# Kernel optimization log

Hardware: AMD Instinct MI355X
Metric: run time of the kernel (lower is better)

Reference implementation:

```python
import jax, jax.numpy as jnp
import numpy as np
import math

N_HEAD = 16
N_EMBED = 1024
BLOCK_SIZE = 2048


def setup_inputs() -> dict:
    key = jax.random.key(0)
    k0, k1, k2, k3, k4 = jax.random.split(key, 5)
    B, T, C = 2, 2048, N_EMBED
    x = jax.random.normal(k0, (B, T, C), dtype=jnp.float32)
    # torch nn.Linear weights: [out_features, in_features]
    s_attn = 1.0 / math.sqrt(C)
    W_attn = jax.random.uniform(k1, (3 * C, C), dtype=jnp.float32, minval=-s_attn, maxval=s_attn)
    b_attn = jax.random.uniform(k2, (3 * C,), dtype=jnp.float32, minval=-s_attn, maxval=s_attn)
    W_proj = jax.random.uniform(k3, (C, C), dtype=jnp.float32, minval=-s_attn, maxval=s_attn)
    b_proj = jax.random.uniform(k4, (C,), dtype=jnp.float32, minval=-s_attn, maxval=s_attn)
    return {"x": x, "W_attn": W_attn, "b_attn": b_attn, "W_proj": W_proj, "b_proj": b_proj}


def reference(x, W_attn, b_attn, W_proj, b_proj):
    B, T, C = x.shape
    H = N_HEAD
    D = C // H
    qkv = x @ W_attn.T + b_attn                     # [B,T,3C]
    q, k, v = jnp.split(qkv, 3, axis=2)
    # [B,T,C] -> [B,H,T,D]
    q = q.reshape(B, T, H, D).transpose(0, 2, 1, 3)
    k = k.reshape(B, T, H, D).transpose(0, 2, 1, 3)
    v = v.reshape(B, T, H, D).transpose(0, 2, 1, 3)
    scale = 1.0 / math.sqrt(D)
    attn = jnp.einsum('bhqd,bhkd->bhqk', q, k) * scale   # [B,H,T,T]
    causal = jnp.tril(jnp.ones((T, T), dtype=bool))
    attn = jnp.where(causal[None, None, :, :], attn, -jnp.inf)
    attn = jax.nn.softmax(attn, axis=-1)
    y = jnp.einsum('bhqk,bhkd->bhqd', attn, v)           # [B,H,T,D]
    y = y.transpose(0, 2, 1, 3).reshape(B, T, C)
    return y @ W_proj.T + b_proj
```

## Files before the change

### kernel.cpp

```cpp
#include <hip/hip_runtime.h>
#include <hip/hip_bf16.h>

#define B_  2
#define T_  2048
#define C_  1024
#define H_  16
#define D_  64
#define M_  (B_*T_)
#define N1_ (3*C_)

typedef short bf16x8 __attribute__((ext_vector_type(8)));
typedef short bf16x4 __attribute__((ext_vector_type(4)));
typedef float f32x4 __attribute__((ext_vector_type(4)));
typedef unsigned short u16;
typedef u16 u16x8 __attribute__((ext_vector_type(8)));

#define QSCALE 0.18033688011112042f
#define C8     11.541560327111707f

__device__ __forceinline__ u16 f2bf(float f) {
  unsigned u = __float_as_uint(f);
  u += 0x7FFFu + ((u >> 16) & 1u);
  return (u16)(u >> 16);
}

__device__ __forceinline__ void gload16(const void* g, void* l) {
  __builtin_amdgcn_global_load_lds((__attribute__((address_space(1))) void*)g,
                                   (__attribute__((address_space(3))) void*)l,
                                   16, 0, 0);
}

__global__ __launch_bounds__(256) void cvt3(const float* __restrict__ x,
                                            const float* __restrict__ wa,
                                            const float* __restrict__ wp,
                                            u16* __restrict__ out) {
  int i = (blockIdx.x * 256 + threadIdx.x) * 8;
  const float* src;
  int off;
  if (i < M_ * C_)                 { src = x;  off = 0; }
  else if (i < M_ * C_ + N1_ * C_) { src = wa; off = M_ * C_; }
  else                             { src = wp; off = M_ * C_ + N1_ * C_; }
  float4 a = *(const float4*)(src + (i - off));
  float4 b = *(const float4*)(src + (i - off) + 4);
  u16x8 o;
  o[0] = f2bf(a.x); o[1] = f2bf(a.y); o[2] = f2bf(a.z); o[3] = f2bf(a.w);
  o[4] = f2bf(b.x); o[5] = f2bf(b.y); o[6] = f2bf(b.z); o[7] = f2bf(b.w);
  *(u16x8*)(out + i) = o;
}

__device__ __forceinline__ void gemm_core(const u16* __restrict__ A,
                                          const u16* __restrict__ W,
                                          u16* As, u16* Bs,
                                          f32x4 (&acc)[4][4],
                                          int m0, int n0, int K) {
  int tid = threadIdx.x;
  int lane = tid & 63, wid = tid >> 6;
  int wr = wid >> 1, wc = wid & 1;

  int arow = wid * 16 + (lane >> 2);
  int ag = lane & 3;
  int sg = ag ^ ((arow >> 1) & 3);
  const u16* aSrc0 = A + (m0 + arow) * K + sg * 8;
  const u16* aSrc1 = aSrc0 + 64 * K;
  const u16* bSrc0 = W + (n0 + arow) * K + sg * 8;
  const u16* bSrc1 = bSrc0 + 64 * K;
  u16* aDst0 = As + (wid * 16) * 32;
  u16* aDst1 = As + (64 + wid * 16) * 32;
  u16* bDst0 = Bs + (wid * 16) * 32;
  u16* bDst1 = Bs + (64 + wid * 16) * 32;

  int rg = lane >> 4;
  int aoff[4], boff[4];
#pragma unroll
  for (int m = 0; m < 4; ++m) {
    int row = wr * 64 + m * 16 + (lane & 15);
    aoff[m] = row * 32 + (rg ^ ((row >> 1) & 3)) * 8;
    row = wc * 64 + m * 16 + (lane & 15);
    boff[m] = row * 32 + (rg ^ ((row >> 1) & 3)) * 8;
  }

  for (int kt = 0; kt < K / 32; ++kt) {
    int k0 = kt * 32;
    __syncthreads();
    gload16(aSrc0 + k0, aDst0);
    gload16(aSrc1 + k0, aDst1);
    gload16(bSrc0 + k0, bDst0);
    gload16(bSrc1 + k0, bDst1);
    __syncthreads();

    bf16x8 af[4], bfr[4];
#pragma unroll
    for (int m = 0; m < 4; ++m) af[m] = *(const bf16x8*)(As + aoff[m]);
#pragma unroll
    for (int n = 0; n < 4; ++n) bfr[n] = *(const bf16x8*)(Bs + boff[n]);
#pragma unroll
    for (int m = 0; m < 4; ++m)
#pragma unroll
      for (int n = 0; n < 4; ++n)
        acc[m][n] = __builtin_amdgcn_mfma_f32_16x16x32_bf16(af[m], bfr[n], acc[m][n], 0, 0, 0);
  }
}

__global__ __launch_bounds__(256) void gemm_qkv(const u16* __restrict__ A,
                                                const u16* __restrict__ W,
                                                const float* __restrict__ bias,
                                                u16* __restrict__ Qb,
                                                u16* __restrict__ Kb,
                                                u16* __restrict__ Vt) {
  __shared__ __align__(16) u16 As[128 * 32];
  __shared__ __align__(16) u16 Bs[128 * 32];
  f32x4 acc[4][4] = {};
  int m0 = blockIdx.x * 128, n0 = blockIdx.y * 128;
  gemm_core(A, W, As, Bs, acc, m0, n0, C_);

  int lane = threadIdx.x & 63, wid = threadIdx.x >> 6;
  int wr = wid >> 1, wc = wid & 1;
  int rg = lane >> 4, cl = lane & 15;
#pragma unroll
  for (int n = 0; n < 4; ++n) {
    int gn = n0 + wc * 64 + n * 16 + cl;
    float bv = bias[gn];
    int seg = gn >> 10, cc = gn & 1023;
    int h = cc >> 6, d = cc & 63;
    float sc = (seg == 0) ? QSCALE : 1.0f;
#pragma unroll
    for (int m = 0; m < 4; ++m) {
#pragma unroll
      for (int r = 0; r < 4; ++r) {
        int gm = m0 + wr * 64 + m * 16 + rg * 4 + r;
        int b = gm >> 11, t = gm & 2047;
        u16 val = f2bf((acc[m][n][r] + bv) * sc);
        int bh = b * 16 + h;
        if (seg == 0)      Qb[(bh * 2048 + t) * 64 + d] = val;
        else if (seg == 1) Kb[(bh * 2048 + t) * 64 + d] = val;
        else               Vt[(bh * 64 + d) * 2048 + t] = val;
      }
    }
  }
}

__global__ __launch_bounds__(256) void gemm_proj(const u16* __restrict__ A,
                                                 const u16* __restrict__ W,
                                                 const float* __restrict__ bias,
                                                 float* __restrict__ out) {
  __shared__ __align__(16) u16 As[128 * 32];
  __shared__ __align__(16) u16 Bs[128 * 32];
  f32x4 acc[4][4] = {};
  int m0 = blockIdx.x * 128, n0 = blockIdx.y * 128;
  gemm_core(A, W, As, Bs, acc, m0, n0, C_);

  int lane = threadIdx.x & 63, wid = threadIdx.x >> 6;
  int wr = wid >> 1, wc = wid & 1;
  int rg = lane >> 4, cl = lane & 15;
#pragma unroll
  for (int n = 0; n < 4; ++n) {
    int gn = n0 + wc * 64 + n * 16 + cl;
    float bv = bias[gn];
#pragma unroll
    for (int m = 0; m < 4; ++m) {
#pragma unroll
      for (int r = 0; r < 4; ++r) {
        int gm = m0 + wr * 64 + m * 16 + rg * 4 + r;
        out[gm * 1024 + gn] = acc[m][n][r] + bv;
      }
    }
  }
}

__global__ __launch_bounds__(128, 2) void attn_fwd(const u16* __restrict__ Qb,
                                                   const u16* __restrict__ Kb,
                                                   const u16* __restrict__ Vt,
                                                   u16* __restrict__ Yb) {
  __shared__ __align__(16) u16 Ps[2][32 * 64];
  __shared__ __align__(16) f32x4 Co[8][64];
  __shared__ float Cl[2][64];
  int tid = threadIdx.x, lane = tid & 63, wid = tid >> 6;
  int cl = lane & 15, kg = lane >> 4;
  int bid = blockIdx.x;
  int bh = bid & 31;
  int qwi = 63 - (bid >> 5);
  int qw0 = qwi * 32;
  int jmax = qwi >> 1;
  int fc0 = wid * 2;
  const u16* Qp = Qb + (size_t)bh * (2048 * 64);
  const u16* Kp = Kb + (size_t)bh * (2048 * 64);
  const u16* Vp = Vt + (size_t)bh * (64 * 2048);
  u16* Pw = Ps[wid];

  int kbase = cl * 64 + kg * 8 + fc0 * 1024;
  int vbase = cl * 2048 + wid * 32 + kg * 8;

  bf16x8 qf[2][2];
#pragma unroll
  for (int fr = 0; fr < 2; ++fr)
#pragma unroll
    for (int dk = 0; dk < 2; ++dk)
      qf[fr][dk] = *(const bf16x8*)(Qp + (qw0 + fr * 16 + cl) * 64 + dk * 32 + kg * 8);

  f32x4 o[2][4] = {};
  float lsum[2] = {0.f, 0.f};
  const f32x4 CINIT = {-C8, -C8, -C8, -C8};

  auto LOADK = [&](bf16x8 (&kf)[2][2], int j) {
    const u16* Kj = Kp + j * 4096 + kbase;
#pragma unroll
    for (int fcl = 0; fcl < 2; ++fcl) {
      kf[fcl][0] = *(const bf16x8*)(Kj + fcl * 1024);
      kf[fcl][1] = *(const bf16x8*)(Kj + fcl * 1024 + 32);
    }
  };

  auto LOADV = [&](bf16x8 (&vf)[4], int j) {
    const u16* Vj = Vp + j * 64 + vbase;
#pragma unroll
    for (int dc = 0; dc < 4; ++dc)
      vf[dc] = *(const bf16x8*)(Vj + dc * 32768);
  };

  auto CORE = [&](bf16x8 (&kf)[2][2], bf16x8 (&vf)[4], int j, bool edge) {
    f32x4 s[2][2];
#pragma unroll
    for (int fcl = 0; fcl < 2; ++fcl)
#pragma unroll
      for (int fr = 0; fr < 2; ++fr) {
        f32x4 z = CINIT;
        z = __builtin_amdgcn_mfma_f32_16x16x32_bf16(kf[fcl][0], qf[fr][0], z, 0, 0, 0);
        z = __builtin_amdgcn_mfma_f32_16x16x32_bf16(kf[fcl][1], qf[fr][1], z, 0, 0, 0);
        s[fr][fcl] = z;
      }
    if (edge) {
#pragma unroll
      for (int fr = 0; fr < 2; ++fr) {
        int qg = qw0 + fr * 16 + cl;
#pragma unroll
        for (int fcl = 0; fcl < 2; ++fcl)
#pragma unroll
          for (int r = 0; r < 4; ++r)
            if (j * 64 + (fc0 + fcl) * 16 + kg * 4 + r > qg) s[fr][fcl][r] = -1e30f;
      }
    }

#pragma unroll
    for (int fr = 0; fr < 2; ++fr) {
      int rowb = (fr * 16 + cl) * 64;
#pragma unroll
      for (int fcl = 0; fcl < 2; ++fcl) {
        float p0 = exp2f(s[fr][fcl][0]);
        float p1 = exp2f(s[fr][fcl][1]);
        float p2 = exp2f(s[fr][fcl][2]);
        float p3 = exp2f(s[fr][fcl][3]);
        lsum[fr] += (p0 + p1) + (p2 + p3);
        union { bf16x4 v; __hip_bfloat162 h[2]; } pk;
        pk.h[0] = __float22bfloat162_rn(make_float2(p0, p1));
        pk.h[1] = __float22bfloat162_rn(make_float2(p2, p3));
        int fc = fc0 + fcl;
        *(bf16x4*)(Pw + rowb + (((fc * 2 + (kg >> 1)) ^ (cl & 7)) * 8) + (kg & 1) * 4) = pk.v;
      }
    }
#pragma unroll
    for (int fr = 0; fr < 2; ++fr) {
      int rowb = (fr * 16 + cl) * 64;
      bf16x8 pf = *(const bf16x8*)(Pw + rowb + (((wid * 4 + kg) ^ (cl & 7)) * 8));
#pragma unroll
      for (int dc = 0; dc < 4; ++dc)
        o[fr][dc] = __builtin_amdgcn_mfma_f32_16x16x32_bf16(pf, vf[dc], o[fr][dc], 0, 0, 0);
    }
  };

  bool edgeMine = (fc0 <= ((qwi & 1) ? 3 : 1));

  bf16x8 kA[2][2], kB[2][2], vA[4], vB[4];
  LOADK(kA, 0); LOADV(vA, 0);
  if (jmax == 0) {
    if (edgeMine) CORE(kA, vA, 0, true);
  } else {
    LOADK(kB, 1); LOADV(vB, 1);
    int j = 0;
    while (j + 1 < jmax) {
      CORE(kA, vA, j, false);
      LOADK(kA, j + 2); LOADV(vA, j + 2);
      CORE(kB, vB, j + 1, false);
      int nx = (j + 3 <= jmax) ? j + 3 : jmax;
      LOADK(kB, nx); LOADV(vB, nx);
      j += 2;
    }
    if (j < jmax) { CORE(kA, vA, j, false); if (edgeMine) CORE(kB, vB, jmax, true); }
    else          { if (edgeMine) CORE(kA, vA, jmax, true); }
  }

  if (wid == 1) {
#pragma unroll
    for (int fr = 0; fr < 2; ++fr) {
      Cl[fr][lane] = lsum[fr];
#pragma unroll
      for (int dc = 0; dc < 4; ++dc) Co[fr * 4 + dc][lane] = o[fr][dc];
    }
  }
  __syncthreads();
  if (wid == 0) {
    int b = bh >> 4, h = bh & 15;
#pragma unroll
    for (int fr = 0; fr < 2; ++fr) {
      float l = lsum[fr] + Cl[fr][lane];
#pragma unroll
      for (int dc = 0; dc < 4; ++dc) o[fr][dc] += Co[fr * 4 + dc][lane];
      l += __shfl_xor(l, 16);
      l += __shfl_xor(l, 32);
      float linv = 1.f / l;
      float li[4];
#pragma unroll
      for (int r = 0; r < 4; ++r) li[r] = __shfl(linv, kg * 4 + r);
#pragma unroll
      for (int dc = 0; dc < 4; ++dc)
#pragma unroll
        for (int r = 0; r < 4; ++r) {
          int t = qw0 + fr * 16 + kg * 4 + r;
          int d = dc * 16 + cl;
          Yb[((size_t)(b * 2048 + t)) * 1024 + h * 64 + d] = f2bf(o[fr][dc][r] * li[r]);
        }
    }
  }
}

extern "C" void kernel_launch(void* const* d_in, const int* in_sizes, int n_in,
                              void* d_out, int out_size, void* d_ws, size_t ws_size,
                              hipStream_t stream) {
  const float* x  = (const float*)d_in[0];
  const float* Wa = (const float*)d_in[1];
  const float* ba = (const float*)d_in[2];
  const float* Wp = (const float*)d_in[3];
  const float* bp = (const float*)d_in[4];
  float* out = (float*)d_out;

  u16* xb  = (u16*)d_ws;
  u16* Wab = xb  + (size_t)M_ * C_;
  u16* Wpb = Wab + (size_t)N1_ * C_;
  u16* Qb  = Wpb + (size_t)C_ * C_;
  u16* Kb  = Qb  + (size_t)M_ * C_;
  u16* Vt  = Kb  + (size_t)M_ * C_;
  u16* Yb  = Vt  + (size_t)M_ * C_;

  cvt3<<<(M_ * C_ + N1_ * C_ + C_ * C_) / 2048, 256, 0, stream>>>(x, Wa, Wp, xb);
  gemm_qkv<<<dim3(M_ / 128, N1_ / 128), 256, 0, stream>>>(xb, Wab, ba, Qb, Kb, Vt);
  attn_fwd<<<2048, 128, 0, stream>>>(Qb, Kb, Vt, Yb);
  gemm_proj<<<dim3(M_ / 128, C_ / 128), 256, 0, stream>>>(Yb, Wpb, bp, out);
}
```

Measured before the change: 137.1 us.

## Split attention core into score/exp and PV phases with double-buffered P

```diff
diff --git a/kernel.cpp b/kernel.cpp
--- a/kernel.cpp
+++ b/kernel.cpp
@@ -171,7 +171,7 @@
                                                    const u16* __restrict__ Kb,
                                                    const u16* __restrict__ Vt,
                                                    u16* __restrict__ Yb) {
-  __shared__ __align__(16) u16 Ps[2][32 * 64];
+  __shared__ __align__(16) u16 Ps[2][2][32 * 64];
   __shared__ __align__(16) f32x4 Co[8][64];
   __shared__ float Cl[2][64];
   int tid = threadIdx.x, lane = tid & 63, wid = tid >> 6;
@@ -185,7 +185,8 @@
   const u16* Qp = Qb + (size_t)bh * (2048 * 64);
   const u16* Kp = Kb + (size_t)bh * (2048 * 64);
   const u16* Vp = Vt + (size_t)bh * (64 * 2048);
-  u16* Pw = Ps[wid];
+  u16* P0 = Ps[wid][0];
+  u16* P1 = Ps[wid][1];
 
   int kbase = cl * 64 + kg * 8 + fc0 * 1024;
   int vbase = cl * 2048 + wid * 32 + kg * 8;
@@ -217,7 +218,7 @@
       vf[dc] = *(const bf16x8*)(Vj + dc * 32768);
   };
 
-  auto CORE = [&](bf16x8 (&kf)[2][2], bf16x8 (&vf)[4], int j, bool edge) {
+  auto SEXP = [&](bf16x8 (&kf)[2][2], int j, bool edge, u16* Pw) {
     f32x4 s[2][2];
 #pragma unroll
     for (int fcl = 0; fcl < 2; ++fcl)
@@ -239,7 +240,6 @@
             if (j * 64 + (fc0 + fcl) * 16 + kg * 4 + r > qg) s[fr][fcl][r] = -1e30f;
       }
     }
-
 #pragma unroll
     for (int fr = 0; fr < 2; ++fr) {
       int rowb = (fr * 16 + cl) * 64;
@@ -257,6 +257,9 @@
         *(bf16x4*)(Pw + rowb + (((fc * 2 + (kg >> 1)) ^ (cl & 7)) * 8) + (kg & 1) * 4) = pk.v;
       }
     }
+  };
+
+  auto PV = [&](bf16x8 (&vf)[4], u16* Pw) {
 #pragma unroll
     for (int fr = 0; fr < 2; ++fr) {
       int rowb = (fr * 16 + cl) * 64;
@@ -269,23 +272,30 @@
 
   bool edgeMine = (fc0 <= ((qwi & 1) ? 3 : 1));
 
-  bf16x8 kA[2][2], kB[2][2], vA[4], vB[4];
-  LOADK(kA, 0); LOADV(vA, 0);
-  if (jmax == 0) {
-    if (edgeMine) CORE(kA, vA, 0, true);
+  bf16x8 k0[2][2], k1[2][2], v0[4], v1[4];
+  LOADK(k0, 0);
+  if (jmax >= 1) LOADK(k1, 1);
+
+  int j = 0;
+  while (j + 1 < jmax) {
+    LOADV(v0, j);
+    LOADV(v1, j + 1);
+    SEXP(k0, j, false, P0);
+    SEXP(k1, j + 1, false, P1);
+    LOADK(k0, j + 2);
+    LOADK(k1, (j + 3 <= jmax) ? j + 3 : jmax);
+    PV(v0, P0);
+    PV(v1, P1);
+    j += 2;
+  }
+  if (j == jmax) {
+    if (edgeMine) { LOADV(v0, j); SEXP(k0, j, true, P0); PV(v0, P0); }
   } else {
-    LOADK(kB, 1); LOADV(vB, 1);
-    int j = 0;
-    while (j + 1 < jmax) {
-      CORE(kA, vA, j, false);
-      LOADK(kA, j + 2); LOADV(vA, j + 2);
-      CORE(kB, vB, j + 1, false);
-      int nx = (j + 3 <= jmax) ? j + 3 : jmax;
-      LOADK(kB, nx); LOADV(vB, nx);
-      j += 2;
-    }
-    if (j < jmax) { CORE(kA, vA, j, false); if (edgeMine) CORE(kB, vB, jmax, true); }
-    else          { if (edgeMine) CORE(kA, vA, jmax, true); }
+    LOADV(v0, j);
+    SEXP(k0, j, false, P0);
+    if (edgeMine) { LOADV(v1, j + 1); SEXP(k1, j + 1, true, P1); }
+    PV(v0, P0);
+    if (edgeMine) PV(v1, P1);
   }
 
   if (wid == 1) {
```

Measured after the change: 136.8 us. Within noise of the previous version (-0.2%).

## Share LDS-staged K/V tiles across four query groups in attention kernel

Applied to the files above, without the earlier changes.

```diff
diff --git a/kernel.cpp b/kernel.cpp
--- a/kernel.cpp
+++ b/kernel.cpp
@@ -60,10 +60,10 @@
   int arow = wid * 16 + (lane >> 2);
   int ag = lane & 3;
   int sg = ag ^ ((arow >> 1) & 3);
-  const u16* aSrc0 = A + (m0 + arow) * K + sg * 8;
-  const u16* aSrc1 = aSrc0 + 64 * K;
-  const u16* bSrc0 = W + (n0 + arow) * K + sg * 8;
-  const u16* bSrc1 = bSrc0 + 64 * K;
+  const u16* aSrc0 = A + (size_t)(m0 + arow) * K + sg * 8;
+  const u16* aSrc1 = aSrc0 + (size_t)64 * K;
+  const u16* bSrc0 = W + (size_t)(n0 + arow) * K + sg * 8;
+  const u16* bSrc1 = bSrc0 + (size_t)64 * K;
   u16* aDst0 = As + (wid * 16) * 32;
   u16* aDst1 = As + (64 + wid * 16) * 32;
   u16* bDst0 = Bs + (wid * 16) * 32;
@@ -131,9 +131,9 @@
         int b = gm >> 11, t = gm & 2047;
         u16 val = f2bf((acc[m][n][r] + bv) * sc);
         int bh = b * 16 + h;
-        if (seg == 0)      Qb[(bh * 2048 + t) * 64 + d] = val;
-        else if (seg == 1) Kb[(bh * 2048 + t) * 64 + d] = val;
-        else               Vt[(bh * 64 + d) * 2048 + t] = val;
+        if (seg == 0)      Qb[((size_t)(bh * 2048 + t)) * 64 + d] = val;
+        else if (seg == 1) Kb[((size_t)(bh * 2048 + t)) * 64 + d] = val;
+        else               Vt[((size_t)(bh * 64 + d)) * 2048 + t] = val;
       }
     }
   }
@@ -161,63 +161,73 @@
 #pragma unroll
       for (int r = 0; r < 4; ++r) {
         int gm = m0 + wr * 64 + m * 16 + rg * 4 + r;
-        out[gm * 1024 + gn] = acc[m][n][r] + bv;
-      }
-    }
-  }
-}
-
-__global__ __launch_bounds__(128, 2) void attn_fwd(const u16* __restrict__ Qb,
+        out[(size_t)gm * 1024 + gn] = acc[m][n][r] + bv;
+      }
+    }
+  }
+}
+
+__global__ __launch_bounds__(512, 2) void attn_fwd(const u16* __restrict__ Qb,
                                                    const u16* __restrict__ Kb,
                                                    const u16* __restrict__ Vt,
                                                    u16* __restrict__ Yb) {
-  __shared__ __align__(16) u16 Ps[2][32 * 64];
-  __shared__ __align__(16) f32x4 Co[8][64];
-  __shared__ float Cl[2][64];
-  int tid = threadIdx.x, lane = tid & 63, wid = tid >> 6;
+  __shared__ __align__(16) u16 Ks[2][64 * 64];
+  __shared__ __align__(16) u16 Vs[2][64 * 64];
+  __shared__ __align__(16) u16 Ps[8][32 * 32];
+  int tid = threadIdx.x, lane = tid & 63, w = tid >> 6;
+  int w4 = w >> 1, kvh = w & 1;
   int cl = lane & 15, kg = lane >> 4;
+  int sw = (cl ^ (cl >> 2)) & 3;
   int bid = blockIdx.x;
   int bh = bid & 31;
-  int qwi = 63 - (bid >> 5);
-  int qw0 = qwi * 32;
-  int jmax = qwi >> 1;
-  int fc0 = wid * 2;
+  int i = bid >> 5;
+  int qt = (i < 8) ? i : 23 - i;
+  int qb0 = qt * 128 + w4 * 32;
+  int jmaxw = (qb0 + 31) >> 6;
+  int jmaxb = 2 * qt + 1;
+  bool hasHigh = (qb0 & 32) != 0;
   const u16* Qp = Qb + (size_t)bh * (2048 * 64);
   const u16* Kp = Kb + (size_t)bh * (2048 * 64);
   const u16* Vp = Vt + (size_t)bh * (64 * 2048);
-  u16* Pw = Ps[wid];
-
-  int kbase = cl * 64 + kg * 8 + fc0 * 1024;
-  int vbase = cl * 2048 + wid * 32 + kg * 8;
+  u16* Pw = Ps[w];
+
+  int srow8 = lane >> 3;
+  int sg = (lane & 7) ^ srow8;
+  const u16* Ksrc = Kp + (w * 8 + srow8) * 64 + sg * 8;
+  const u16* Vsrc = Vp + (w * 8 + srow8) * 2048 + sg * 8;
 
   bf16x8 qf[2][2];
 #pragma unroll
   for (int fr = 0; fr < 2; ++fr)
 #pragma unroll
     for (int dk = 0; dk < 2; ++dk)
-      qf[fr][dk] = *(const bf16x8*)(Qp + (qw0 + fr * 16 + cl) * 64 + dk * 32 + kg * 8);
+      qf[fr][dk] = *(const bf16x8*)(Qp + (qb0 + fr * 16 + cl) * 64 + dk * 32 + kg * 8);
 
   f32x4 o[2][4] = {};
   float lsum[2] = {0.f, 0.f};
   const f32x4 CINIT = {-C8, -C8, -C8, -C8};
 
-  auto LOADK = [&](bf16x8 (&kf)[2][2], int j) {
-    const u16* Kj = Kp + j * 4096 + kbase;
+  auto STAGE = [&](int j, int buf) {
+    gload16(Ksrc + j * 4096, &Ks[buf][w * 512]);
+    gload16(Vsrc + j * 64, &Vs[buf][w * 512]);
+  };
+
+  auto CORE = [&](int buf, int j, bool mask) {
+    const u16* Kl = Ks[buf];
+    const u16* Vl = Vs[buf];
+    bf16x8 kf[2][2];
 #pragma unroll
     for (int fcl = 0; fcl < 2; ++fcl) {
-      kf[fcl][0] = *(const bf16x8*)(Kj + fcl * 1024);
-      kf[fcl][1] = *(const bf16x8*)(Kj + fcl * 1024 + 32);
-    }
-  };
-
-  auto LOADV = [&](bf16x8 (&vf)[4], int j) {
-    const u16* Vj = Vp + j * 64 + vbase;
-#pragma unroll
-    for (int dc = 0; dc < 4; ++dc)
-      vf[dc] = *(const bf16x8*)(Vj + dc * 32768);
-  };
-
-  auto CORE = [&](bf16x8 (&kf)[2][2], bf16x8 (&vf)[4], int j, bool edge) {
+      int row = (kvh * 2 + fcl) * 16 + cl;
+      kf[fcl][0] = *(const bf16x8*)(Kl + row * 64 + ((kg ^ (cl & 7)) * 8));
+      kf[fcl][1] = *(const bf16x8*)(Kl + row * 64 + (((4 + kg) ^ (cl & 7)) * 8));
+    }
+    bf16x8 vf[4];
+#pragma unroll
+    for (int dc = 0; dc < 4; ++dc) {
+      int row = dc * 16 + cl;
+      vf[dc] = *(const bf16x8*)(Vl + row * 64 + (((kvh * 4 + kg) ^ (cl & 7)) * 8));
+    }
     f32x4 s[2][2];
 #pragma unroll
     for (int fcl = 0; fcl < 2; ++fcl)
@@ -228,21 +238,20 @@
         z = __builtin_amdgcn_mfma_f32_16x16x32_bf16(kf[fcl][1], qf[fr][1], z, 0, 0, 0);
         s[fr][fcl] = z;
       }
-    if (edge) {
+    if (mask) {
 #pragma unroll
       for (int fr = 0; fr < 2; ++fr) {
-        int qg = qw0 + fr * 16 + cl;
+        int qg = qb0 + fr * 16 + cl;
 #pragma unroll
         for (int fcl = 0; fcl < 2; ++fcl)
 #pragma unroll
           for (int r = 0; r < 4; ++r)
-            if (j * 64 + (fc0 + fcl) * 16 + kg * 4 + r > qg) s[fr][fcl][r] = -1e30f;
-      }
-    }
-
+            if (j * 64 + (kvh * 2 + fcl) * 16 + kg * 4 + r > qg) s[fr][fcl][r] = -1e30f;
+      }
+    }
 #pragma unroll
     for (int fr = 0; fr < 2; ++fr) {
-      int rowb = (fr * 16 + cl) * 64;
+      int rowb = (fr * 16 + cl) * 32;
 #pragma unroll
       for (int fcl = 0; fcl < 2; ++fcl) {
         float p0 = exp2f(s[fr][fcl][0]);
@@ -253,57 +262,49 @@
         union { bf16x4 v; __hip_bfloat162 h[2]; } pk;
         pk.h[0] = __float22bfloat162_rn(make_float2(p0, p1));
         pk.h[1] = __float22bfloat162_rn(make_float2(p2, p3));
-        int fc = fc0 + fcl;
-        *(bf16x4*)(Pw + rowb + (((fc * 2 + (kg >> 1)) ^ (cl & 7)) * 8) + (kg & 1) * 4) = pk.v;
-      }
-    }
+        *(bf16x4*)(Pw + rowb + (((fcl * 2 + (kg >> 1)) ^ sw) * 8) + (kg & 1) * 4) = pk.v;
+      }
+    }
+    bf16x8 pf[2];
+#pragma unroll
+    for (int fr = 0; fr < 2; ++fr)
+      pf[fr] = *(const bf16x8*)(Pw + (fr * 16 + cl) * 32 + ((kg ^ sw) * 8));
+#pragma unroll
+    for (int fr = 0; fr < 2; ++fr)
+#pragma unroll
+      for (int dc = 0; dc < 4; ++dc)
+        o[fr][dc] = __builtin_amdgcn_mfma_f32_16x16x32_bf16(pf[fr], vf[dc], o[fr][dc], 0, 0, 0);
+  };
+
+  STAGE(0, 0);
+  __syncthreads();
+  int buf = 0;
+  for (int j = 0; j <= jmaxb; ++j) {
+    if (j < jmaxb) STAGE(j + 1, buf ^ 1);
+    if (j < jmaxw)       CORE(buf, j, false);
+    else if (j == jmaxw && (kvh == 0 || hasHigh)) CORE(buf, j, true);
+    __syncthreads();
+    buf ^= 1;
+  }
+
+  f32x4* Co = (f32x4*)((w4 < 2) ? (void*)&Ks[0][0] : (void*)&Vs[0][0]) + (w4 & 1) * 512;
+  float*  Cl = (float*)&Ps[0][0] + w4 * 128;
+  if (kvh == 1) {
 #pragma unroll
     for (int fr = 0; fr < 2; ++fr) {
-      int rowb = (fr * 16 + cl) * 64;
-      bf16x8 pf = *(const bf16x8*)(Pw + rowb + (((wid * 4 + kg) ^ (cl & 7)) * 8));
-#pragma unroll
-      for (int dc = 0; dc < 4; ++dc)
-        o[fr][dc] = __builtin_amdgcn_mfma_f32_16x16x32_bf16(pf, vf[dc], o[fr][dc], 0, 0, 0);
-    }
-  };
-
-  bool edgeMine = (fc0 <= ((qwi & 1) ? 3 : 1));
-
-  bf16x8 kA[2][2], kB[2][2], vA[4], vB[4];
-  LOADK(kA, 0); LOADV(vA, 0);
-  if (jmax == 0) {
-    if (edgeMine) CORE(kA, vA, 0, true);
-  } else {
-    LOADK(kB, 1); LOADV(vB, 1);
-    int j = 0;
-    while (j + 1 < jmax) {
-      CORE(kA, vA, j, false);
-      LOADK(kA, j + 2); LOADV(vA, j + 2);
-      CORE(kB, vB, j + 1, false);
-      int nx = (j + 3 <= jmax) ? j + 3 : jmax;
-      LOADK(kB, nx); LOADV(vB, nx);
-      j += 2;
-    }
-    if (j < jmax) { CORE(kA, vA, j, false); if (edgeMine) CORE(kB, vB, jmax, true); }
-    else          { if (edgeMine) CORE(kA, vA, jmax, true); }
-  }
-
-  if (wid == 1) {
+      Cl[fr * 64 + lane] = lsum[fr];
+#pragma unroll
+      for (int dc = 0; dc < 4; ++dc) Co[(fr * 4 + dc) * 64 + lane] = o[fr][dc];
+    }
+  }
+  __syncthreads();
+  if (kvh == 0) {
+    int b = bh >> 4, h = bh & 15;
 #pragma unroll
     for (int fr = 0; fr < 2; ++fr) {
-      Cl[fr][lane] = lsum[fr];
-#pragma unroll
-      for (int dc = 0; dc < 4; ++dc) Co[fr * 4 + dc][lane] = o[fr][dc];
-    }
-  }
-  __syncthreads();
-  if (wid == 0) {
-    int b = bh >> 4, h = bh & 15;
-#pragma unroll
-    for (int fr = 0; fr < 2; ++fr) {
-      float l = lsum[fr] + Cl[fr][lane];
-#pragma unroll
-      for (int dc = 0; dc < 4; ++dc) o[fr][dc] += Co[fr * 4 + dc][lane];
+      float l = lsum[fr] + Cl[fr * 64 + lane];
+#pragma unroll
+      for (int dc = 0; dc < 4; ++dc) o[fr][dc] += Co[(fr * 4 + dc) * 64 + lane];
       l += __shfl_xor(l, 16);
       l += __shfl_xor(l, 32);
       float linv = 1.f / l;
@@ -314,7 +315,7 @@
       for (int dc = 0; dc < 4; ++dc)
 #pragma unroll
         for (int r = 0; r < 4; ++r) {
-          int t = qw0 + fr * 16 + kg * 4 + r;
+          int t = qb0 + fr * 16 + kg * 4 + r;
           int d = dc * 16 + cl;
           Yb[((size_t)(b * 2048 + t)) * 1024 + h * 64 + d] = f2bf(o[fr][dc][r] * li[r]);
         }
@@ -342,6 +343,6 @@
 
   cvt3<<<(M_ * C_ + N1_ * C_ + C_ * C_) / 2048, 256, 0, stream>>>(x, Wa, Wp, xb);
   gemm_qkv<<<dim3(M_ / 128, N1_ / 128), 256, 0, stream>>>(xb, Wab, ba, Qb, Kb, Vt);
-  attn_fwd<<<2048, 128, 0, stream>>>(Qb, Kb, Vt, Yb);
+  attn_fwd<<<512, 512, 0, stream>>>(Qb, Kb, Vt, Yb);
   gemm_proj<<<dim3(M_ / 128, C_ / 128), 256, 0, stream>>>(Yb, Wpb, bp, out);
 }
```

Result: faster. 112.6 us (-17.8%).
